# Optimization experiments

Measured on AMD Instinct MI355X. Metric: run time of the kernel, lower is better.

## Reference

```python
import jax, jax.numpy as jnp
import numpy as np

B, N, D, H = 4, 2048, 1024, 8
HD = D // H  # head_dim = 128
TEMPER = 1.0
LN_EPS = 1e-5


def setup_inputs() -> dict:
    key = jax.random.key(0)
    ks = jax.random.split(key, 6)
    return {
        "h": jax.random.normal(ks[0], (B, N, D), dtype=jnp.float32),
        "Wl": jax.random.normal(ks[1], (D, D), dtype=jnp.float32) * (D ** -0.5),
        "Wr": jax.random.normal(ks[2], (D, D), dtype=jnp.float32) * (D ** -0.5),
        "att_l": jax.random.normal(ks[3], (1, HD), dtype=jnp.float32) * (HD ** -0.5),
        "att_r": jax.random.normal(ks[4], (1, HD), dtype=jnp.float32) * (HD ** -0.5),
        "Wf": jax.random.normal(ks[5], (D, D), dtype=jnp.float32) * (D ** -0.5),
        "ln_gamma": jnp.ones((D,), dtype=jnp.float32),
        "ln_beta": jnp.zeros((D,), dtype=jnp.float32),
    }


def _leaky(x):
    return jnp.where(x > 0, x, 0.01 * x)


def reference(h, Wl, Wr, att_l, att_r, Wf, ln_gamma, ln_beta):
    b, n, d = h.shape
    # projections -> [B, H, N, HD]
    fl = (h @ Wl.T).reshape(b, n, H, HD).transpose(0, 2, 1, 3)
    fr = (h @ Wr.T).reshape(b, n, H, HD).transpose(0, 2, 1, 3)
    # additive (GAT-style) scores: sl[b,h,i] + sr[b,h,j]
    sl = jnp.einsum("bhnd,d->bhn", _leaky(fl), att_l[0])
    sr = jnp.einsum("bhnd,d->bhn", _leaky(fr), att_r[0])
    score = (sl[:, :, :, None] + sr[:, :, None, :]) / TEMPER  # [B,H,N,N]
    p = jax.nn.softmax(score, axis=-1)
    # context and merge heads
    ctx = jnp.einsum("bhnm,bhmd->bhnd", p, fr)
    h_sa = ctx.transpose(0, 2, 1, 3).reshape(b, n, d)
    fh = h_sa @ Wf.T
    y = h + fh
    mu = jnp.mean(y, axis=-1, keepdims=True)
    var = jnp.mean(jnp.square(y - mu), axis=-1, keepdims=True)
    return (y - mu) * jax.lax.rsqrt(var + LN_EPS) * ln_gamma + ln_beta
```

## Files before the change

kernel.cpp:

```cpp
#include <hip/hip_runtime.h>
#include <hip/hip_bf16.h>

#define B_ 4
#define N_ 2048
#define D_ 1024
#define H_ 8
#define HD_ 128

typedef __attribute__((ext_vector_type(4))) float f32x4;
typedef __attribute__((ext_vector_type(8))) short bf16x8;

__device__ __forceinline__ short f2bf(float f) {
    unsigned u = __builtin_bit_cast(unsigned, f);
    u = (u + 0x7FFFu + ((u >> 16) & 1u)) >> 16;
    return (short)u;
}
__device__ __forceinline__ float bf2f(unsigned short s) {
    unsigned u = (unsigned)s << 16;
    return __builtin_bit_cast(float, u);
}

typedef const __attribute__((address_space(1))) void* gas_t;
typedef __attribute__((address_space(3))) void* las_t;

__device__ __forceinline__ void gload16(const void* g, void* l) {
    __builtin_amdgcn_global_load_lds((gas_t)g, (las_t)l, 16, 0, 0);
}

__global__ __launch_bounds__(256) void k_cvt(
    const float* __restrict__ h, short* __restrict__ hb,
    const float* __restrict__ Wr, short* __restrict__ wrb)
{
    int blk = blockIdx.x;
    const float* src;
    short* dst;
    int i;
    if (blk < 4096) { src = h;  dst = hb;  i = blk * 256 + threadIdx.x; }
    else            { src = Wr; dst = wrb; i = (blk - 4096) * 256 + threadIdx.x; }
    float4 a = ((const float4*)src)[i * 2];
    float4 b = ((const float4*)src)[i * 2 + 1];
    bf16x8 o;
    o[0] = f2bf(a.x); o[1] = f2bf(a.y); o[2] = f2bf(a.z); o[3] = f2bf(a.w);
    o[4] = f2bf(b.x); o[5] = f2bf(b.y); o[6] = f2bf(b.z); o[7] = f2bf(b.w);
    ((bf16x8*)dst)[i] = o;
}

__global__ __launch_bounds__(256) void k_proj_sr(
    const short* __restrict__ hb, const short* __restrict__ wrb,
    const float* __restrict__ att_r, float* __restrict__ sr)
{
    __shared__ short sA[2][64 * 32];
    __shared__ short sB[2][128 * 32];
    __shared__ float part[4][64];

    const int tid  = threadIdx.x;
    const int lane = tid & 63;
    const int wave = tid >> 6;
    const int cc   = lane & 15;
    const int g    = lane >> 4;
    const int rowBase = blockIdx.x * 64;
    const int head    = blockIdx.y;

    const int srow = lane >> 2;
    const int scol = (lane & 3) * 8;
    const short* gA0 = hb  + (size_t)(rowBase + wave * 16 + srow) * D_ + scol;
    const short* gB0 = wrb + (size_t)(head * HD_ + wave * 32 + srow) * D_ + scol;
    const short* gB1 = gB0 + (size_t)16 * D_;
    const int offA = wave * 1024;
    const int offB = wave * 2048;

    f32x4 acc[4][2];
#pragma unroll
    for (int m = 0; m < 4; ++m)
#pragma unroll
        for (int n = 0; n < 2; ++n) acc[m][n] = (f32x4){0.f, 0.f, 0.f, 0.f};

    gload16(gA0, (char*)sA[0] + offA);
    gload16(gB0, (char*)sB[0] + offB);
    gload16(gB1, (char*)sB[0] + offB + 1024);
    __syncthreads();

    for (int t = 0; t < 32; ++t) {
        const int cur = t & 1;
        if (t < 31) {
            const int k0 = (t + 1) * 32;
            gload16(gA0 + k0, (char*)sA[cur ^ 1] + offA);
            gload16(gB0 + k0, (char*)sB[cur ^ 1] + offB);
            gload16(gB1 + k0, (char*)sB[cur ^ 1] + offB + 1024);
        }
        const short* bufA = sA[cur];
        const short* bufB = sB[cur];
        bf16x8 aF[4], bF[2];
#pragma unroll
        for (int m = 0; m < 4; ++m)
            aF[m] = *(const bf16x8*)(bufA + (m * 16 + cc) * 32 + g * 8);
#pragma unroll
        for (int n = 0; n < 2; ++n)
            bF[n] = *(const bf16x8*)(bufB + (wave * 32 + n * 16 + cc) * 32 + g * 8);
        __builtin_amdgcn_s_setprio(1);
#pragma unroll
        for (int m = 0; m < 4; ++m)
#pragma unroll
            for (int n = 0; n < 2; ++n)
                acc[m][n] = __builtin_amdgcn_mfma_f32_16x16x32_bf16(
                    aF[m], bF[n], acc[m][n], 0, 0, 0);
        __builtin_amdgcn_s_setprio(0);
        __syncthreads();
    }

    float ar[2];
#pragma unroll
    for (int n = 0; n < 2; ++n) ar[n] = att_r[wave * 32 + n * 16 + cc];

#pragma unroll
    for (int m = 0; m < 4; ++m) {
#pragma unroll
        for (int r = 0; r < 4; ++r) {
            float p = 0.f;
#pragma unroll
            for (int n = 0; n < 2; ++n) {
                float v = acc[m][n][r];
                v = v > 0.f ? v : 0.01f * v;
                p += v * ar[n];
            }
            p += __shfl_xor(p, 1); p += __shfl_xor(p, 2);
            p += __shfl_xor(p, 4); p += __shfl_xor(p, 8);
            if (cc == 0) part[wave][m * 16 + g * 4 + r] = p;
        }
    }
    __syncthreads();
    if (tid < 64) {
        const int grow = rowBase + tid;
        const int b = grow >> 11, j = grow & (N_ - 1);
        sr[(size_t)(b * H_ + head) * N_ + j] =
            part[0][tid] + part[1][tid] + part[2][tid] + part[3][tid];
    }
}

__global__ __launch_bounds__(256) void k_hbar(
    const short* __restrict__ hbm, const float* __restrict__ sr,
    float* __restrict__ hp)
{
    const int dc = blockIdx.x;
    const int jc = blockIdx.y;
    const int b  = blockIdx.z;
    const int tid = threadIdx.x;
    const int d = dc * 256 + tid;

    __shared__ float smx[8], sism[8];
    {
        const int hh = tid >> 5;
        const int sl = tid & 31;
        const float4* row = (const float4*)(sr + (size_t)(b * H_ + hh) * N_);
        float4 v[16];
        float mx = -1e30f;
#pragma unroll
        for (int k = 0; k < 16; ++k) {
            v[k] = row[sl + k * 32];
            mx = fmaxf(fmaxf(mx, fmaxf(v[k].x, v[k].y)), fmaxf(v[k].z, v[k].w));
        }
#pragma unroll
        for (int m = 1; m < 32; m <<= 1) mx = fmaxf(mx, __shfl_xor(mx, m));
        float sum = 0.f;
#pragma unroll
        for (int k = 0; k < 16; ++k)
            sum += expf(v[k].x - mx) + expf(v[k].y - mx) +
                   expf(v[k].z - mx) + expf(v[k].w - mx);
#pragma unroll
        for (int m = 1; m < 32; m <<= 1) sum += __shfl_xor(sum, m);
        if (sl == 0) { smx[hh] = mx; sism[hh] = 1.f / sum; }
    }
    __syncthreads();

    __shared__ float wl[8][128];
    for (int idx = tid; idx < 1024; idx += 256) {
        const int hh = idx >> 7, jj = idx & 127;
        wl[hh][jj] = expf(sr[(size_t)(b * H_ + hh) * N_ + jc * 128 + jj]
                          - smx[hh]) * sism[hh];
    }
    __syncthreads();

    float acc[8] = {0.f, 0.f, 0.f, 0.f, 0.f, 0.f, 0.f, 0.f};
    const short* hp0 = hbm + ((size_t)(b * N_ + jc * 128)) * D_ + d;
#pragma unroll 4
    for (int jj = 0; jj < 128; ++jj) {
        float hv = bf2f((unsigned short)hp0[(size_t)jj * D_]);
#pragma unroll
        for (int hh = 0; hh < 8; ++hh) acc[hh] += wl[hh][jj] * hv;
    }
#pragma unroll
    for (int hh = 0; hh < 8; ++hh)
        hp[((size_t)(jc * 32) + b * 8 + hh) * D_ + d] = acc[hh];
}

__global__ __launch_bounds__(256) void k_ctx(
    const float* __restrict__ hp, const float* __restrict__ Wr,
    float* __restrict__ ctx)
{
    const int bh = blockIdx.x >> 5;
    const int b = bh >> 3, head = bh & 7;
    const int dg = (blockIdx.x & 31) * 4;
    const int tid = threadIdx.x;
    const int lane = tid & 63, wave = tid >> 6;

    __shared__ float xs[1024];
    float4 s = {0.f, 0.f, 0.f, 0.f};
#pragma unroll
    for (int jc = 0; jc < 16; ++jc) {
        float4 v = ((const float4*)(hp + ((size_t)(jc * 32) + bh) * D_))[tid];
        s.x += v.x; s.y += v.y; s.z += v.z; s.w += v.w;
    }
    ((float4*)xs)[tid] = s;
    __syncthreads();

    const int o = dg + wave;
    const float* wrow = Wr + (size_t)(head * HD_ + o) * D_;
    float acc = 0.f;
#pragma unroll
    for (int it = 0; it < 4; ++it) {
        float4 wv = *(const float4*)(wrow + it * 256 + lane * 4);
        float4 xv = ((const float4*)xs)[it * 64 + lane];
        acc += wv.x * xv.x + wv.y * xv.y + wv.z * xv.z + wv.w * xv.w;
    }
#pragma unroll
    for (int m = 1; m < 64; m <<= 1) acc += __shfl_xor(acc, m);
    if (lane == 0) ctx[(size_t)b * D_ + head * HD_ + o] = acc;
}

__global__ __launch_bounds__(256) void k_fvec(
    const float* __restrict__ ctx, const float* __restrict__ Wf,
    float* __restrict__ fvec)
{
    const int o = blockIdx.x * 4 + (threadIdx.x >> 6);
    const int lane = threadIdx.x & 63;
    const int b = o >> 10, orow = o & 1023;
    const float* x  = ctx + (size_t)b * D_;
    const float* wf = Wf + (size_t)orow * D_;
    float s = 0.f;
#pragma unroll
    for (int it = 0; it < 4; ++it) {
        float4 xv = *(const float4*)(x + it * 256 + lane * 4);
        float4 wv = *(const float4*)(wf + it * 256 + lane * 4);
        s += xv.x * wv.x + xv.y * wv.y + xv.z * wv.z + xv.w * wv.w;
    }
#pragma unroll
    for (int m = 1; m < 64; m <<= 1) s += __shfl_xor(s, m);
    if (lane == 0) fvec[o] = s;
}

__global__ __launch_bounds__(256) void k_ln(
    const short* __restrict__ hbm, const float* __restrict__ fvec,
    const float* __restrict__ gamma, const float* __restrict__ beta,
    float* __restrict__ out)
{
    const int row = blockIdx.x;
    const int b = row >> 11;
    const int tid = threadIdx.x;
    const int lane = tid & 63, wave = tid >> 6;

    short4 hv4 = *(const short4*)(hbm + (size_t)row * D_ + tid * 4);
    float4 fv = *(const float4*)(fvec + (size_t)b * D_ + tid * 4);
    const float y0 = bf2f((unsigned short)hv4.x) + fv.x;
    const float y1 = bf2f((unsigned short)hv4.y) + fv.y;
    const float y2 = bf2f((unsigned short)hv4.z) + fv.z;
    const float y3 = bf2f((unsigned short)hv4.w) + fv.w;

    float s = y0 + y1 + y2 + y3;
    float q = y0 * y0 + y1 * y1 + y2 * y2 + y3 * y3;
#pragma unroll
    for (int m = 1; m < 64; m <<= 1) { s += __shfl_xor(s, m); q += __shfl_xor(q, m); }

    __shared__ float rs[4], rq[4];
    if (lane == 0) { rs[wave] = s; rq[wave] = q; }
    __syncthreads();
    s = rs[0] + rs[1] + rs[2] + rs[3];
    q = rq[0] + rq[1] + rq[2] + rq[3];

    const float mu  = s * (1.f / D_);
    const float var = q * (1.f / D_) - mu * mu;
    const float inv = rsqrtf(var + 1e-5f);

    float4 gv = *(const float4*)(gamma + tid * 4);
    float4 bv = *(const float4*)(beta + tid * 4);
    float4 ov;
    ov.x = (y0 - mu) * inv * gv.x + bv.x;
    ov.y = (y1 - mu) * inv * gv.y + bv.y;
    ov.z = (y2 - mu) * inv * gv.z + bv.z;
    ov.w = (y3 - mu) * inv * gv.w + bv.w;
    *(float4*)(out + (size_t)row * D_ + tid * 4) = ov;
}

extern "C" void kernel_launch(void* const* d_in, const int* in_sizes, int n_in,
                              void* d_out, int out_size, void* d_ws, size_t ws_size,
                              hipStream_t stream) {
    const float* h     = (const float*)d_in[0];
    const float* Wr    = (const float*)d_in[2];
    const float* att_r = (const float*)d_in[4];
    const float* Wf    = (const float*)d_in[5];
    const float* gamma = (const float*)d_in[6];
    const float* beta  = (const float*)d_in[7];
    float* out = (float*)d_out;

    char* ws = (char*)d_ws;
    float* sr    = (float*)(ws);
    float* hp    = (float*)(ws + 524288);
    float* ctx   = (float*)(ws + 2752512);
    float* fvec  = (float*)(ws + 2768896);
    short* hb    = (short*)(ws + 4194304);
    short* wrb   = (short*)(ws + 4194304 + 16777216);

    k_cvt<<<4096 + 512, 256, 0, stream>>>(h, hb, Wr, wrb);
    k_proj_sr<<<dim3(B_ * N_ / 64, H_), 256, 0, stream>>>(hb, wrb, att_r, sr);
    k_hbar<<<dim3(4, 16, 4), 256, 0, stream>>>(hb, sr, hp);
    k_ctx<<<1024, 256, 0, stream>>>(hp, Wr, ctx);
    k_fvec<<<1024, 256, 0, stream>>>(ctx, Wf, fvec);
    k_ln<<<B_ * N_, 256, 0, stream>>>(hb, fvec, gamma, beta, out);
}
```

Measured before the change: 78.20 us.

## Prefetch two K-tiles ahead with partial vmcnt waits in the projection GEMM

Restructures the double-buffered K loop of the projection kernel so two stages are issued up front. Each iteration waits only for the older stage's loads (vmcnt(3)) instead of draining all outstanding loads through __syncthreads. It then refills the freed buffer after a second barrier. The aim is to keep global-to-LDS loads in flight during the MFMA work, at the cost of hand-written waitcnt and barrier ordering that has to stay correct for the direct-to-LDS loads.

```diff
diff --git a/kernel.cpp b/kernel.cpp
--- a/kernel.cpp
+++ b/kernel.cpp
@@ -75,19 +75,12 @@
 #pragma unroll
         for (int n = 0; n < 2; ++n) acc[m][n] = (f32x4){0.f, 0.f, 0.f, 0.f};
 
-    gload16(gA0, (char*)sA[0] + offA);
-    gload16(gB0, (char*)sB[0] + offB);
-    gload16(gB1, (char*)sB[0] + offB + 1024);
-    __syncthreads();
-
-    for (int t = 0; t < 32; ++t) {
-        const int cur = t & 1;
-        if (t < 31) {
-            const int k0 = (t + 1) * 32;
-            gload16(gA0 + k0, (char*)sA[cur ^ 1] + offA);
-            gload16(gB0 + k0, (char*)sB[cur ^ 1] + offB);
-            gload16(gB1 + k0, (char*)sB[cur ^ 1] + offB + 1024);
-        }
+    auto STAGE = [&](int bufidx, int kk) {
+        gload16(gA0 + kk, (char*)sA[bufidx] + offA);
+        gload16(gB0 + kk, (char*)sB[bufidx] + offB);
+        gload16(gB1 + kk, (char*)sB[bufidx] + offB + 1024);
+    };
+    auto COMPUTE = [&](int cur) {
         const short* bufA = sA[cur];
         const short* bufB = sB[cur];
         bf16x8 aF[4], bF[2];
@@ -105,8 +98,24 @@
                 acc[m][n] = __builtin_amdgcn_mfma_f32_16x16x32_bf16(
                     aF[m], bF[n], acc[m][n], 0, 0, 0);
         __builtin_amdgcn_s_setprio(0);
-        __syncthreads();
-    }
+    };
+
+    STAGE(0, 0);
+    STAGE(1, 32);
+
+    for (int t = 0; t < 31; ++t) {
+        asm volatile("s_waitcnt vmcnt(3)" ::: "memory");
+        __builtin_amdgcn_s_barrier();
+        __builtin_amdgcn_sched_barrier(0);
+        COMPUTE(t & 1);
+        __builtin_amdgcn_sched_barrier(0);
+        __builtin_amdgcn_s_barrier();
+        if (t < 30) STAGE(t & 1, (t + 2) * 32);
+    }
+    asm volatile("s_waitcnt vmcnt(0)" ::: "memory");
+    __builtin_amdgcn_s_barrier();
+    __builtin_amdgcn_sched_barrier(0);
+    COMPUTE(1);
 
     float ar[2];
 #pragma unroll
```

Result: no change. 78.27 us (+0.1%).
